# Performance work log

Measured on AMD Instinct MI355X. Metric: run time of the kernel, lower is better.

The kernel has to match this reference:

```python
import jax, jax.numpy as jnp
import numpy as np
import math

B, N, C, H = 32, 512, 768, 12
HD = C // H
KEEP_RATE = 0.7
SCALE = HD ** -0.5
BOUNDARY = math.ceil(KEEP_RATE * (N - 1))  # 358


def setup_inputs() -> dict:
    key = jax.random.key(0)
    k1, k2, k3, k4 = jax.random.split(key, 4)
    x = jax.random.normal(k1, (B, N, C), jnp.float32) * 0.02
    # prefix (left-aligned) key-padding mask: valid length per sample in [N//4, N]
    lengths = jax.random.randint(k2, (B,), N // 4, N + 1)
    key_mask = (jnp.arange(N)[None, :] < lengths[:, None])  # [B, N]
    attn_mask = jnp.broadcast_to(key_mask[:, None, :], (B, N, N)).astype(jnp.int32)
    w_qkv = jax.random.normal(k3, (C, 3 * C), jnp.float32) * (C ** -0.5)
    w_proj = jax.random.normal(k4, (C, C), jnp.float32) * (C ** -0.5)
    b_proj = jnp.zeros((C,), jnp.float32)
    return {"x": x, "attn_mask": attn_mask, "w_qkv": w_qkv, "w_proj": w_proj, "b_proj": b_proj}


def reference(x, attn_mask, w_qkv, w_proj, b_proj):
    # qkv projection and head split: [B,N,3C] -> [3,B,H,N,HD]
    qkv = (x @ w_qkv).reshape(B, N, 3, H, HD).transpose(2, 0, 3, 1, 4)
    q, k, v = qkv[0], qkv[1], qkv[2]
    attn = jnp.einsum('bhqd,bhkd->bhqk', q, k) * SCALE          # [B,H,N,N]
    mask4 = attn_mask[:, None, :, :]                            # broadcast over heads
    attn = jnp.where(mask4 == 0, jnp.float32(-1e9), attn)
    attn = jax.nn.softmax(attn, axis=-1)
    out = jnp.einsum('bhqk,bhkd->bhqd', attn, v)                # [B,H,N,HD]
    out = out.transpose(0, 2, 1, 3).reshape(B, N, C)
    out = out @ w_proj + b_proj

    # per-sample top-k token pruning based on CLS attention (keep_rate < 1)
    key_row = attn_mask[:, 0, 1:]                               # [B, N-1] key padding row
    cls_mean = attn[:, :, 0, 1:].mean(axis=1)                   # mean over heads, [B, N-1]
    valid = key_row != 0
    scores = jnp.where(valid, cls_mean, -jnp.inf)
    valid_count = valid.sum(axis=1)                             # [B]
    left = jnp.ceil(valid_count.astype(jnp.float32) * KEEP_RATE).astype(jnp.int32)
    _, top_idx = jax.lax.top_k(scores, BOUNDARY)                # sorted desc, [B, BOUNDARY]
    pos = jnp.arange(BOUNDARY)[None, :]
    # slots beyond per-sample left_tokens are padded with 1e9 (matches torch cat padding)
    idx = jnp.where(pos < left[:, None], top_idx.astype(jnp.float32), jnp.float32(1e9))
    index = jnp.broadcast_to(idx[:, :, None], (B, BOUNDARY, C))
    return (out, index, idx, BOUNDARY)
```

## Files before the change

kernel.cpp:

```cpp
#include <hip/hip_runtime.h>
#include <hip/hip_bf16.h>

#define Bb 32
#define Nn 512
#define Cc 768
#define Hh 12
#define HDd 64
#define BND 358
#define QS 0.18033688f

typedef unsigned short u16;
typedef unsigned int u32;
typedef __attribute__((ext_vector_type(8))) short bf16x8;
typedef __attribute__((ext_vector_type(4))) float f32x4;
typedef __attribute__((ext_vector_type(16))) float f32x16;
typedef __attribute__((ext_vector_type(4))) int i32x4;

__device__ __forceinline__ f32x4 MFMA16(bf16x8 a, bf16x8 b, f32x4 c) {
  return __builtin_amdgcn_mfma_f32_16x16x32_bf16(a, b, c, 0, 0, 0);
}
__device__ __forceinline__ f32x16 MFMA32(bf16x8 a, bf16x8 b, f32x16 c) {
  return __builtin_amdgcn_mfma_f32_32x32x16_bf16(a, b, c, 0, 0, 0);
}

__device__ __forceinline__ u32 f2bf(float f) {
  u32 u = __builtin_bit_cast(u32, f);
  return (u + 0x7fffu + ((u >> 16) & 1u)) >> 16;
}
__device__ __forceinline__ u32 packbf2(float a, float b) { return f2bf(a) | (f2bf(b) << 16); }
__device__ __forceinline__ u32 cvtpk2(float a, float b) {
  float2 f2 = {a, b};
  __hip_bfloat162 h = __float22bfloat162_rn(f2);
  u32 r;
  __builtin_memcpy(&r, &h, 4);
  return r;
}
__device__ __forceinline__ float bf2f(u16 h) { return __builtin_bit_cast(float, (u32)h << 16); }

__device__ __forceinline__ void async_copy16(void* lds, const void* g) {
  __builtin_amdgcn_global_load_lds((const __attribute__((address_space(1))) void*)g,
                                   (__attribute__((address_space(3))) void*)lds, 16, 0, 0);
}


__global__ __launch_bounds__(256) void k_convx(const float* __restrict__ x, u16* __restrict__ xb) {
  int gid = blockIdx.x * 256 + threadIdx.x;
  if (gid >= (Bb * Nn * Cc) / 4) return;
  float4 v = *(const float4*)&x[gid * 4];
  u32 p0 = packbf2(v.x, v.y), p1 = packbf2(v.z, v.w);
  uint2 st = {p0, p1};
  *(uint2*)&xb[gid * 4] = st;
}

__global__ __launch_bounds__(256) void k_transpose(const float* __restrict__ src, u16* __restrict__ dst,
                                                   int R, int Ccols) {
  __shared__ float tbuf[32][33];
  int c0 = blockIdx.x * 32, r0 = blockIdx.y * 32;
  int lx = threadIdx.x & 31, ly = threadIdx.x >> 5;
  #pragma unroll
  for (int rr = ly; rr < 32; rr += 8) tbuf[rr][lx] = src[(long)(r0 + rr) * Ccols + c0 + lx];
  __syncthreads();
  #pragma unroll
  for (int cc = ly; cc < 32; cc += 8) dst[(long)(c0 + cc) * R + r0 + lx] = (u16)f2bf(tbuf[lx][cc]);
}

__global__ __launch_bounds__(256) void k_lens(const int* __restrict__ mask, int* __restrict__ lens) {
  int b = blockIdx.x, t = threadIdx.x;
  __shared__ int red[256];
  red[t] = mask[(long)b * Nn * Nn + t] + mask[(long)b * Nn * Nn + t + 256];
  __syncthreads();
  for (int s = 128; s > 0; s >>= 1) {
    if (t < s) red[t] += red[t + s];
    __syncthreads();
  }
  if (t == 0) lens[b] = red[0];
}

template <int MODE, int SWAP>
__global__ __launch_bounds__(256) void k_gemm2(const u16* __restrict__ A, const u16* __restrict__ Bt,
                                               int nb0, u16* __restrict__ Qo, u16* __restrict__ Ko,
                                               u16* __restrict__ Vto, float* __restrict__ Co,
                                               const float* __restrict__ bias) {
  __shared__ u16 As[2][128 * 64];
  __shared__ u16 Bs[2][128 * 64];
  int m0 = blockIdx.x * 128;
  int nb = nb0 + blockIdx.y * 128;
  int t = threadIdx.x, lane = t & 63, wave = t >> 6;
  int wr = wave >> 1, wc = wave & 1;
  int qlane = lane & 15, g = lane >> 4;
  f32x4 acc[4][4] = {};

  auto stage = [&](int kt, int buf) {
    #pragma unroll
    for (int i = 0; i < 4; ++i) {
      int chunk = i * 256 + t;
      int row = chunk >> 3;
      int cp = (chunk & 7) << 4;
      int src = cp ^ ((row & 7) << 4);
      const u16* ga = A + (long)(m0 + row) * 768 + kt * 64 + (src >> 1);
      const u16* gb = Bt + (long)(nb + row) * 768 + kt * 64 + (src >> 1);
      async_copy16(&As[buf][(i * 256 + wave * 64) * 8], ga);
      async_copy16(&Bs[buf][(i * 256 + wave * 64) * 8], gb);
    }
  };

  auto compute = [&](int buf) {
    #pragma unroll
    for (int kk = 0; kk < 2; ++kk) {
      bf16x8 af[4], bf[4];
      #pragma unroll
      for (int x = 0; x < 4; ++x) {
        int ra = wr * 64 + x * 16 + qlane;
        int ca = (kk * 64 + g * 16) ^ ((ra & 7) << 4);
        af[x] = *(const bf16x8*)&As[buf][ra * 64 + (ca >> 1)];
        int rb = wc * 64 + x * 16 + qlane;
        int cb = (kk * 64 + g * 16) ^ ((rb & 7) << 4);
        bf[x] = *(const bf16x8*)&Bs[buf][rb * 64 + (cb >> 1)];
      }
      #pragma unroll
      for (int mi = 0; mi < 4; ++mi)
        #pragma unroll
        for (int ni = 0; ni < 4; ++ni)
          acc[mi][ni] = SWAP ? MFMA16(bf[ni], af[mi], acc[mi][ni])
                             : MFMA16(af[mi], bf[ni], acc[mi][ni]);
    }
  };

  stage(0, 0);
  __syncthreads();
  int cur = 0;
  for (int kt = 0; kt < 12; ++kt) {
    if (kt < 11) stage(kt + 1, cur ^ 1);
    compute(cur);
    __syncthreads();
    cur ^= 1;
  }

  if (MODE == 0 && SWAP == 1) {
    #pragma unroll
    for (int mi = 0; mi < 4; ++mi) {
      int m = m0 + wr * 64 + mi * 16 + qlane;
      int b = m >> 9, qi = m & 511;
      #pragma unroll
      for (int ni = 0; ni < 4; ++ni) {
        int nf = nb + wc * 64 + ni * 16 + g * 4;
        int which = nf >= 768;
        int rem = nf - which * 768;
        int hh = rem >> 6, d0 = rem & 63;
        u16* dst = (which ? Ko : Qo) + ((long)(b * Hh + hh) * Nn + qi) * HDd + d0;
        float sc = which ? 1.f : QS;
        uint2 st = {packbf2(acc[mi][ni][0] * sc, acc[mi][ni][1] * sc),
                    packbf2(acc[mi][ni][2] * sc, acc[mi][ni][3] * sc)};
        *(uint2*)dst = st;
      }
    }
  } else if (MODE == 0) {
    #pragma unroll
    for (int mi = 0; mi < 4; ++mi) {
      int m = m0 + wr * 64 + mi * 16 + g * 4;
      int b = m >> 9, qi = m & 511;
      #pragma unroll
      for (int ni = 0; ni < 4; ++ni) {
        int rem = nb + wc * 64 + ni * 16 + qlane - 1536;
        int hh = rem >> 6, d = rem & 63;
        u16* dst = Vto + (long)(b * Hh + hh) * (Nn * HDd) + (qi >> 5) * 2048 + d * 32 + (qi & 31);
        uint2 st = {packbf2(acc[mi][ni][0], acc[mi][ni][1]),
                    packbf2(acc[mi][ni][2], acc[mi][ni][3])};
        *(uint2*)dst = st;
      }
    }
  } else {
    #pragma unroll
    for (int mi = 0; mi < 4; ++mi) {
      #pragma unroll
      for (int ni = 0; ni < 4; ++ni) {
        int n = nb + wc * 64 + ni * 16 + qlane;
        float bv = bias[n];
        #pragma unroll
        for (int r = 0; r < 4; ++r) {
          int m = m0 + wr * 64 + mi * 16 + g * 4 + r;
          Co[(long)m * Cc + n] = acc[mi][ni][r] + bv;
        }
      }
    }
  }
}

__global__ __launch_bounds__(64) void k_attn(const u16* __restrict__ Q, const u16* __restrict__ K,
                                             const u16* __restrict__ Vt, const int* __restrict__ lens,
                                             u16* __restrict__ AO) {
  int lane = threadIdx.x;
  int bid = blockIdx.x;
  int chunk = bid & 7, h = (bid >> 3) % Hh, b = bid / 96;
  int q0w = chunk * 64;
  int ln = lane & 31, hi = lane >> 5;
  int len = lens[b];
  int nt = (len + 31) >> 5;

  const u16* Qb = Q + (long)(b * Hh + h) * Nn * HDd;
  const u16* Kb = K + (long)(b * Hh + h) * Nn * HDd;
  const u16* Vb = Vt + (long)(b * Hh + h) * Nn * HDd;

  bf16x8 qf[2][4];
  #pragma unroll
  for (int qt = 0; qt < 2; ++qt)
    #pragma unroll
    for (int ds = 0; ds < 4; ++ds)
      qf[qt][ds] = *(const bf16x8*)(Qb + (q0w + qt * 32 + ln) * HDd + ds * 16 + hi * 8);

  f32x16 o[2][2] = {};
  float l[2] = {0.f, 0.f};

  #pragma unroll 1
  for (int t = 0; t < nt; ++t) {
    int k0 = t * 32;
    bf16x8 kf[4], vf[2][2];
    #pragma unroll
    for (int ds = 0; ds < 4; ++ds)
      kf[ds] = *(const bf16x8*)(Kb + (k0 + ln) * HDd + ds * 16 + hi * 8);
    #pragma unroll
    for (int dt = 0; dt < 2; ++dt)
      #pragma unroll
      for (int ks = 0; ks < 2; ++ks)
        vf[dt][ks] = *(const bf16x8*)(Vb + t * 2048 + (dt * 32 + ln) * 32 + ks * 16 + hi * 8);

    bool bdry = (k0 + 32 > len);
    int khi = k0 + 4 * hi;

    #pragma unroll
    for (int qt = 0; qt < 2; ++qt) {
      f32x16 st = {};
      #pragma unroll
      for (int ds = 0; ds < 4; ++ds) st = MFMA32(kf[ds], qf[qt][ds], st);
      if (bdry) {
        #pragma unroll
        for (int r = 0; r < 16; ++r) {
          int key = khi + (r & 3) + 8 * (r >> 2);
          if (key >= len) st[r] = -1e9f;
        }
      }
      float p[16];
      #pragma unroll
      for (int r = 0; r < 16; ++r) p[r] = exp2f(st[r]);
      l[qt] += (((p[0] + p[1]) + (p[2] + p[3])) + ((p[4] + p[5]) + (p[6] + p[7]))) +
               (((p[8] + p[9]) + (p[10] + p[11])) + ((p[12] + p[13]) + (p[14] + p[15])));
      u32 wA0 = cvtpk2(p[0], p[1]), wA1 = cvtpk2(p[2], p[3]);
      u32 wA2 = cvtpk2(p[4], p[5]), wA3 = cvtpk2(p[6], p[7]);
      asm volatile("v_permlane32_swap_b32 %0, %1" : "+v"(wA0), "+v"(wA2));
      asm volatile("v_permlane32_swap_b32 %0, %1" : "+v"(wA1), "+v"(wA3));
      u32 wB0 = cvtpk2(p[8], p[9]), wB1 = cvtpk2(p[10], p[11]);
      u32 wB2 = cvtpk2(p[12], p[13]), wB3 = cvtpk2(p[14], p[15]);
      asm volatile("v_permlane32_swap_b32 %0, %1" : "+v"(wB0), "+v"(wB2));
      asm volatile("v_permlane32_swap_b32 %0, %1" : "+v"(wB1), "+v"(wB3));
      i32x4 bi0 = {(int)wA0, (int)wA1, (int)wA2, (int)wA3};
      i32x4 bi1 = {(int)wB0, (int)wB1, (int)wB2, (int)wB3};
      bf16x8 pb0 = __builtin_bit_cast(bf16x8, bi0);
      bf16x8 pb1 = __builtin_bit_cast(bf16x8, bi1);
      #pragma unroll
      for (int dt = 0; dt < 2; ++dt) {
        o[qt][dt] = MFMA32(vf[dt][0], pb0, o[qt][dt]);
        o[qt][dt] = MFMA32(vf[dt][1], pb1, o[qt][dt]);
      }
    }
  }

  #pragma unroll
  for (int qt = 0; qt < 2; ++qt) {
    float ls = l[qt] + __shfl_xor(l[qt], 32);
    float inv = 1.f / ls;
    u16* outp = AO + ((long)(b * Nn + q0w + qt * 32 + ln) * Cc) + h * HDd;
    #pragma unroll
    for (int dt = 0; dt < 2; ++dt) {
      #pragma unroll
      for (int qd = 0; qd < 4; ++qd) {
        uint2 st2 = {cvtpk2(o[qt][dt][4 * qd + 0] * inv, o[qt][dt][4 * qd + 1] * inv),
                     cvtpk2(o[qt][dt][4 * qd + 2] * inv, o[qt][dt][4 * qd + 3] * inv)};
        *(uint2*)(outp + dt * 32 + 8 * qd + 4 * hi) = st2;
      }
    }
  }
}

__global__ __launch_bounds__(256) void k_sco_init(float* __restrict__ sco) {
  int gid = blockIdx.x * 256 + threadIdx.x;
  if (gid < Bb * 511) sco[gid] = 0.f;
}

__global__ __launch_bounds__(256) void k_cls(const u16* __restrict__ Q, const u16* __restrict__ K,
                                             const int* __restrict__ lens, float* __restrict__ scores) {
  int bh = blockIdx.x;
  int b = bh / Hh;
  int t = threadIdx.x;
  int len = lens[b];
  __shared__ float qrow[64];
  __shared__ float red[256];
  const u16* Qb = Q + (long)bh * Nn * HDd;
  const u16* Kb = K + (long)bh * Nn * HDd;
  if (t < 64) qrow[t] = bf2f(Qb[t]);
  __syncthreads();
  const bf16x8* kr0 = (const bf16x8*)(Kb + t * HDd);
  const bf16x8* kr1 = (const bf16x8*)(Kb + (t + 256) * HDd);
  float d0 = 0.f, d1 = 0.f;
  #pragma unroll
  for (int c8 = 0; c8 < 8; ++c8) {
    bf16x8 kv0 = kr0[c8], kv1 = kr1[c8];
    #pragma unroll
    for (int j = 0; j < 8; ++j) {
      float qv = qrow[c8 * 8 + j];
      d0 += qv * bf2f((u16)kv0[j]);
      d1 += qv * bf2f((u16)kv1[j]);
    }
  }
  float l0 = (t < len) ? d0 : -1e9f;
  float l1 = (t + 256 < len) ? d1 : -1e9f;
  red[t] = fmaxf(l0, l1);
  __syncthreads();
  for (int ss = 128; ss > 0; ss >>= 1) {
    if (t < ss) red[t] = fmaxf(red[t], red[t + ss]);
    __syncthreads();
  }
  float mx = red[0];
  __syncthreads();
  float e0 = exp2f(l0 - mx), e1 = exp2f(l1 - mx);
  red[t] = e0 + e1;
  __syncthreads();
  for (int ss = 128; ss > 0; ss >>= 1) {
    if (t < ss) red[t] += red[t + ss];
    __syncthreads();
  }
  float w = (1.f / 12.f) / red[0];
  if (t >= 1) atomicAdd(&scores[b * 511 + (t - 1)], e0 * w);
  atomicAdd(&scores[b * 511 + (t + 255)], e1 * w);
}

__device__ __forceinline__ bool sless(float sa, int ia, float sb, int ib) {
  return (sa > sb) || (sa == sb && ia < ib);
}

__global__ __launch_bounds__(256) void k_topk(const float* __restrict__ scores,
                                              const int* __restrict__ lens, float* __restrict__ dout) {
  int b = blockIdx.x, t = threadIdx.x;
  __shared__ float sc[512];
  __shared__ int id[512];
  float ninf = -__builtin_inff();
  int len = lens[b];
  for (int i = t; i < 512; i += 256) {
    sc[i] = (i < 511 && (i + 1) < len) ? scores[b * 511 + i] : ninf;
    id[i] = i;
  }
  for (int k = 2; k <= 512; k <<= 1) {
    for (int j = k >> 1; j > 0; j >>= 1) {
      __syncthreads();
      for (int i = t; i < 512; i += 256) {
        int ixj = i ^ j;
        if (ixj > i) {
          float si = sc[i], sj = sc[ixj];
          int ii = id[i], ij = id[ixj];
          bool up = ((i & k) == 0);
          bool dosw = up ? sless(sj, ij, si, ii) : sless(si, ii, sj, ij);
          if (dosw) {
            sc[i] = sj; sc[ixj] = si;
            id[i] = ij; id[ixj] = ii;
          }
        }
      }
    }
  }
  __syncthreads();
  int left = (int)ceilf((float)(len - 1) * 0.7f);
  const long OFF_IDX = (long)Bb * Nn * Cc + (long)Bb * BND * Cc;
  for (int p = t; p < BND; p += 256) {
    dout[OFF_IDX + (long)b * BND + p] = (p < left) ? (float)id[p] : 1e9f;
  }
  if (b == 0 && t == 0) dout[OFF_IDX + (long)Bb * BND] = (float)BND;
}

__global__ __launch_bounds__(256) void k_bcast(float* __restrict__ dout) {
  long gid = (long)blockIdx.x * 256 + threadIdx.x;
  const long total = (long)Bb * BND * (Cc / 4);
  if (gid >= total) return;
  long bp = gid / (Cc / 4);
  int c4 = (int)(gid % (Cc / 4));
  const long OFF_INDEX = (long)Bb * Nn * Cc;
  const long OFF_IDX = OFF_INDEX + (long)Bb * BND * Cc;
  float v = dout[OFF_IDX + bp];
  float4 f = {v, v, v, v};
  *(float4*)&dout[OFF_INDEX + bp * Cc + (long)c4 * 4] = f;
}

extern "C" void kernel_launch(void* const* d_in, const int* in_sizes, int n_in,
                              void* d_out, int out_size, void* d_ws, size_t ws_size,
                              hipStream_t stream) {
  const float* x = (const float*)d_in[0];
  const int* mask = (const int*)d_in[1];
  const float* wqkv = (const float*)d_in[2];
  const float* wproj = (const float*)d_in[3];
  const float* bproj = (const float*)d_in[4];
  float* out = (float*)d_out;

  char* ws = (char*)d_ws;
  u16* Qw  = (u16*)(ws);
  u16* Kw  = (u16*)(ws + 25165824L);
  u16* Vtw = (u16*)(ws + 50331648L);
  u16* XB  = (u16*)(ws + 75497472L);
  u16* AO  = XB;
  u16* WQT = (u16*)(ws + 100663296L);
  u16* WPT = (u16*)(ws + 104202240L);
  float* SCO = (float*)(ws + 105381888L);
  int* LEN = (int*)(ws + 105447424L);

  k_convx<<<12288, 256, 0, stream>>>(x, XB);
  k_transpose<<<dim3(72, 24), 256, 0, stream>>>(wqkv, WQT, 768, 2304);
  k_transpose<<<dim3(24, 24), 256, 0, stream>>>(wproj, WPT, 768, 768);
  k_lens<<<32, 256, 0, stream>>>(mask, LEN);
  k_sco_init<<<64, 256, 0, stream>>>(SCO);
  k_gemm2<0, 1><<<dim3(128, 12), 256, 0, stream>>>(XB, WQT, 0, Qw, Kw, nullptr, nullptr, nullptr);
  k_gemm2<0, 0><<<dim3(128, 6), 256, 0, stream>>>(XB, WQT, 1536, nullptr, nullptr, Vtw, nullptr, nullptr);
  k_attn<<<3072, 64, 0, stream>>>(Qw, Kw, Vtw, LEN, AO);
  k_gemm2<1, 0><<<dim3(128, 6), 256, 0, stream>>>(AO, WPT, 0, nullptr, nullptr, nullptr, out, bproj);
  k_cls<<<384, 256, 0, stream>>>(Qw, Kw, LEN, SCO);
  k_topk<<<32, 256, 0, stream>>>(SCO, LEN, out);
  k_bcast<<<8592, 256, 0, stream>>>(out);
}
```

Baseline: 236.3 us.

## Reorder attention blocks by sequence length and double-buffer K/V tile loads

Adds a tiny kernel that sorts batch samples by valid length and interleaves longest with shortest. The attention grid is remapped so blocks are issued in that balanced order, with the query chunk index outermost. The attention inner loop is also software-pipelined: K/V fragments for the next key tile are loaded into a second register set while the current tile is computed. The aim is to cut load imbalance from variable-length samples and hide global-load latency, at the cost of more registers and an extra serial launch.

```diff
diff --git a/kernel.cpp b/kernel.cpp
--- a/kernel.cpp
+++ b/kernel.cpp
@@ -74,6 +74,20 @@
     __syncthreads();
   }
   if (t == 0) lens[b] = red[0];
+}
+
+__global__ void k_order(const int* __restrict__ lens, int* __restrict__ ord) {
+  if (threadIdx.x == 0 && blockIdx.x == 0) {
+    int idx[32];
+    for (int i = 0; i < 32; ++i) idx[i] = i;
+    for (int i = 1; i < 32; ++i) {
+      int v = idx[i], lv = lens[v], j = i - 1;
+      while (j >= 0 && lens[idx[j]] < lv) { idx[j + 1] = idx[j]; --j; }
+      idx[j + 1] = v;
+    }
+    for (int s = 0; s < 32; ++s)
+      ord[s] = (s & 1) ? idx[31 - (s >> 1)] : idx[s >> 1];
+  }
 }
 
 template <int MODE, int SWAP>
@@ -188,10 +202,13 @@
 
 __global__ __launch_bounds__(64) void k_attn(const u16* __restrict__ Q, const u16* __restrict__ K,
                                              const u16* __restrict__ Vt, const int* __restrict__ lens,
-                                             u16* __restrict__ AO) {
+                                             const int* __restrict__ ord, u16* __restrict__ AO) {
   int lane = threadIdx.x;
   int bid = blockIdx.x;
-  int chunk = bid & 7, h = (bid >> 3) % Hh, b = bid / 96;
+  int bh = bid % (Bb * Hh);
+  int chunk = bid / (Bb * Hh);
+  int b = ord[bh / Hh];
+  int h = bh % Hh;
   int q0w = chunk * 64;
   int ln = lane & 31, hi = lane >> 5;
   int len = lens[b];
@@ -211,10 +228,8 @@
   f32x16 o[2][2] = {};
   float l[2] = {0.f, 0.f};
 
-  #pragma unroll 1
-  for (int t = 0; t < nt; ++t) {
+  auto loadt = [&](bf16x8 (&kf)[4], bf16x8 (&vf)[2][2], int t) {
     int k0 = t * 32;
-    bf16x8 kf[4], vf[2][2];
     #pragma unroll
     for (int ds = 0; ds < 4; ++ds)
       kf[ds] = *(const bf16x8*)(Kb + (k0 + ln) * HDd + ds * 16 + hi * 8);
@@ -223,10 +238,12 @@
       #pragma unroll
       for (int ks = 0; ks < 2; ++ks)
         vf[dt][ks] = *(const bf16x8*)(Vb + t * 2048 + (dt * 32 + ln) * 32 + ks * 16 + hi * 8);
-
+  };
+
+  auto compute = [&](const bf16x8 (&kf)[4], const bf16x8 (&vf)[2][2], int t) {
+    int k0 = t * 32;
     bool bdry = (k0 + 32 > len);
     int khi = k0 + 4 * hi;
-
     #pragma unroll
     for (int qt = 0; qt < 2; ++qt) {
       f32x16 st = {};
@@ -262,7 +279,19 @@
         o[qt][dt] = MFMA32(vf[dt][1], pb1, o[qt][dt]);
       }
     }
-  }
+  };
+
+  bf16x8 kfA[4], vfA[2][2], kfB[4], vfB[2][2];
+  loadt(kfA, vfA, 0);
+  int t = 0;
+  #pragma unroll 1
+  for (; t + 2 <= nt; t += 2) {
+    loadt(kfB, vfB, t + 1);
+    compute(kfA, vfA, t);
+    if (t + 2 < nt) loadt(kfA, vfA, t + 2);
+    compute(kfB, vfB, t + 1);
+  }
+  if (t < nt) compute(kfA, vfA, t);
 
   #pragma unroll
   for (int qt = 0; qt < 2; ++qt) {
@@ -408,15 +437,17 @@
   u16* WPT = (u16*)(ws + 104202240L);
   float* SCO = (float*)(ws + 105381888L);
   int* LEN = (int*)(ws + 105447424L);
+  int* ORD = (int*)(ws + 105447552L);
 
   k_convx<<<12288, 256, 0, stream>>>(x, XB);
   k_transpose<<<dim3(72, 24), 256, 0, stream>>>(wqkv, WQT, 768, 2304);
   k_transpose<<<dim3(24, 24), 256, 0, stream>>>(wproj, WPT, 768, 768);
   k_lens<<<32, 256, 0, stream>>>(mask, LEN);
+  k_order<<<1, 64, 0, stream>>>(LEN, ORD);
   k_sco_init<<<64, 256, 0, stream>>>(SCO);
   k_gemm2<0, 1><<<dim3(128, 12), 256, 0, stream>>>(XB, WQT, 0, Qw, Kw, nullptr, nullptr, nullptr);
   k_gemm2<0, 0><<<dim3(128, 6), 256, 0, stream>>>(XB, WQT, 1536, nullptr, nullptr, Vtw, nullptr, nullptr);
-  k_attn<<<3072, 64, 0, stream>>>(Qw, Kw, Vtw, LEN, AO);
+  k_attn<<<3072, 64, 0, stream>>>(Qw, Kw, Vtw, LEN, ORD, AO);
   k_gemm2<1, 0><<<dim3(128, 6), 256, 0, stream>>>(AO, WPT, 0, nullptr, nullptr, nullptr, out, bproj);
   k_cls<<<384, 256, 0, stream>>>(Qw, Kw, LEN, SCO);
   k_topk<<<32, 256, 0, stream>>>(SCO, LEN, out);
```

New measurement: 265.4 us. +12.3%, slower.
